# Kernel optimization log

Measured on AMD Instinct MI355X. Metric: run time of the kernel, lower is better.

Reference implementation:

```python
import jax, jax.numpy as jnp
import numpy as np

B, N, D = 16, 1024, 768
H = 12
HD = D // H
HID = 4 * D
EPS = 1e-6


def _layernorm(x, g, b):
    mu = jnp.mean(x, axis=-1, keepdims=True)
    var = jnp.mean(jnp.square(x - mu), axis=-1, keepdims=True)
    return (x - mu) * jax.lax.rsqrt(var + EPS) * g + b


def setup_inputs() -> dict:
    key = jax.random.key(0)
    ks = jax.random.split(key, 8)
    s_d = 1.0 / np.sqrt(D)
    s_h = 1.0 / np.sqrt(HID)
    return {
        "x": jax.random.normal(ks[0], (B, N, D), dtype=jnp.float32),
        "qkv_w": jax.random.uniform(ks[1], (3 * D, D), jnp.float32, -s_d, s_d),
        "proj_w": jax.random.uniform(ks[2], (D, D), jnp.float32, -s_d, s_d),
        "proj_b": jax.random.uniform(ks[3], (D,), jnp.float32, -s_d, s_d),
        "fc1_w": jax.random.uniform(ks[4], (HID, D), jnp.float32, -s_d, s_d),
        "fc1_b": jax.random.uniform(ks[5], (HID,), jnp.float32, -s_d, s_d),
        "fc2_w": jax.random.uniform(ks[6], (D, HID), jnp.float32, -s_h, s_h),
        "fc2_b": jax.random.uniform(ks[7], (D,), jnp.float32, -s_h, s_h),
        "norm1_g": jnp.ones((D,), jnp.float32),
        "norm1_b": jnp.zeros((D,), jnp.float32),
        "norm2_g": jnp.ones((D,), jnp.float32),
        "norm2_b": jnp.zeros((D,), jnp.float32),
    }


def _attention(x, qkv_w, proj_w, proj_b):
    b, n, _ = x.shape
    qkv = x @ qkv_w.T                                  # [b,n,3D] (no bias: qkv_bias=False)
    qkv = qkv.reshape(b, n, 3, H, HD)
    q, k, v = (jnp.transpose(qkv[:, :, i], (0, 2, 1, 3)) for i in range(3))  # [b,h,n,hd]
    scale = HD ** (-0.5)
    dots = jnp.einsum("bhid,bhjd->bhij", q, k) * scale
    attn = jax.nn.softmax(dots, axis=-1)
    out = jnp.einsum("bhij,bhjd->bhid", attn, v)
    out = jnp.transpose(out, (0, 2, 1, 3)).reshape(b, n, H * HD)
    return out @ proj_w.T + proj_b


def _mlp(x, fc1_w, fc1_b, fc2_w, fc2_b):
    h = jax.nn.gelu(x @ fc1_w.T + fc1_b, approximate=False)
    return h @ fc2_w.T + fc2_b


def reference(x, qkv_w, proj_w, proj_b, fc1_w, fc1_b, fc2_w, fc2_b,
              norm1_g, norm1_b, norm2_g, norm2_b):
    x = x + _attention(_layernorm(x, norm1_g, norm1_b), qkv_w, proj_w, proj_b)
    x = x + _mlp(_layernorm(x, norm2_g, norm2_b), fc1_w, fc1_b, fc2_w, fc2_b)
    return x
```

## Files before the change

### kernel.cpp

```cpp
#include <hip/hip_runtime.h>
#include <hip/hip_bf16.h>
#include <math.h>

using bf16 = __hip_bfloat16;
typedef __attribute__((ext_vector_type(8))) short short8;
typedef __attribute__((ext_vector_type(4))) short shortx4;
typedef __attribute__((ext_vector_type(4))) float floatx4;

#define BB 16
#define NN 1024
#define DD 768
#define HH 12
#define HD 64
#define HID 3072

#define QSCALE 0.1803368801f

__device__ __forceinline__ floatx4 mfma_bf16(short8 a, short8 b, floatx4 c) {
  return __builtin_amdgcn_mfma_f32_16x16x32_bf16(a, b, c, 0, 0, 0);
}

__device__ __forceinline__ short bf16_bits(float f) {
  union { bf16 h; short s; } u;
  u.h = __float2bfloat16(f);
  return u.s;
}

__device__ __forceinline__ void async_copy16(const void* g, void* l) {
  __builtin_amdgcn_global_load_lds(
      (const __attribute__((address_space(1))) unsigned int*)g,
      (__attribute__((address_space(3))) unsigned int*)l,
      16, 0, 0);
}

__device__ __forceinline__ float gelu_f(float x) {
  const float z = x * fmaf(0.10294324f, x * x, 2.3022082f);
  const float e = exp2f(z);
  return x - x * __builtin_amdgcn_rcpf(e + 1.0f);
}

__global__ __launch_bounds__(256)
void cvt_kernel(const float* __restrict__ in, bf16* __restrict__ out, int n4)
{
  const int i = blockIdx.x * 256 + threadIdx.x;
  if (i >= n4) return;
  const float4 v = ((const float4*)in)[i];
  shortx4 o;
  o.x = bf16_bits(v.x); o.y = bf16_bits(v.y);
  o.z = bf16_bits(v.z); o.w = bf16_bits(v.w);
  ((shortx4*)out)[i] = o;
}

__global__ __launch_bounds__(256)
void ln_kernel(const float* __restrict__ x, const float* __restrict__ g,
               const float* __restrict__ b, bf16* __restrict__ y)
{
  const int row = blockIdx.x;
  const int t = threadIdx.x;
  const float* xr = x + (size_t)row * DD;
  float v[3];
  float s = 0.f, s2 = 0.f;
#pragma unroll
  for (int i = 0; i < 3; ++i) {
    float f = xr[t + i * 256];
    v[i] = f;
    s += f;
    s2 += f * f;
  }
#pragma unroll
  for (int off = 1; off < 64; off <<= 1) {
    s  += __shfl_xor(s, off);
    s2 += __shfl_xor(s2, off);
  }
  __shared__ float red[2][4];
  const int wave = t >> 6, lane = t & 63;
  if (lane == 0) { red[0][wave] = s; red[1][wave] = s2; }
  __syncthreads();
  s  = red[0][0] + red[0][1] + red[0][2] + red[0][3];
  s2 = red[1][0] + red[1][1] + red[1][2] + red[1][3];
  const float mu = s * (1.f / DD);
  const float var = s2 * (1.f / DD) - mu * mu;
  const float inv = rsqrtf(var + 1e-6f);
  bf16* yr = y + (size_t)row * DD;
#pragma unroll
  for (int i = 0; i < 3; ++i) {
    int c = t + i * 256;
    yr[c] = __float2bfloat16((v[i] - mu) * inv * g[c] + b[c]);
  }
}

template <int EPI>
__global__ __launch_bounds__(256, 4)
void gemm_kernel(const bf16* __restrict__ A, const bf16* __restrict__ W,
                 const float* __restrict__ bias, const float* __restrict__ res,
                 void* __restrict__ Cv, int N, int K)
{
  __shared__ __align__(16) short smem[16896];
  short* sA = smem;
  short* sB = smem + 8192;

  const int tid  = threadIdx.x;
  const int lane = tid & 63;
  const int wave = tid >> 6;
  const int wm = wave & 1, wn = wave >> 1;
  const int row16 = lane & 15, quad = lane >> 4;

  const int lin = blockIdx.y * gridDim.x + blockIdx.x;
  const int per = gridDim.x * 8;
  const int pan = lin / per, rem = lin % per;
  const int bm = (pan * 8 + (rem & 7)) * 128;
  const int bn = (rem >> 3) * 128;

  const int lrow = lane >> 3;
  const int lkc  = (lane & 7) ^ lrow;

  const bf16* Ag = A + (size_t)(bm + wave * 32 + lrow) * K + lkc * 8;
  const bf16* Bg = W + (size_t)(bn + wave * 32 + lrow) * K + lkc * 8;
  short* sAw = sA + wave * 2048;
  short* sBw = sB + wave * 2048;

  floatx4 acc[4][4] = {};

  for (int kt = 0; kt < K; kt += 64) {
#pragma unroll
    for (int g = 0; g < 4; ++g) {
      async_copy16(Ag + (size_t)g * 8 * K + kt, sAw + g * 512);
      async_copy16(Bg + (size_t)g * 8 * K + kt, sBw + g * 512);
    }
    __syncthreads();
#pragma unroll
    for (int c = 0; c < 2; ++c) {
      short8 af[4], bfr[4];
      const int kc = c * 4 + quad;
#pragma unroll
      for (int mt = 0; mt < 4; ++mt) {
        const int row = wm * 64 + mt * 16 + row16;
        af[mt] = *(const short8*)&sA[(row >> 3) * 512 + ((row & 7) * 8 + (kc ^ (row & 7))) * 8];
      }
#pragma unroll
      for (int nt = 0; nt < 4; ++nt) {
        const int row = wn * 64 + nt * 16 + row16;
        bfr[nt] = *(const short8*)&sB[(row >> 3) * 512 + ((row & 7) * 8 + (kc ^ (row & 7))) * 8];
      }
#pragma unroll
      for (int mt = 0; mt < 4; ++mt)
#pragma unroll
        for (int nt = 0; nt < 4; ++nt)
          acc[mt][nt] = mfma_bf16(bfr[nt], af[mt], acc[mt][nt]);
    }
    __syncthreads();
  }

  if (EPI == 1) {
#pragma unroll
    for (int mt = 0; mt < 4; ++mt) {
      const int row = bm + wm * 64 + mt * 16 + row16;
#pragma unroll
      for (int nt = 0; nt < 4; ++nt) {
        const int col = bn + wn * 64 + nt * 16 + quad * 4;
        const floatx4 bv = *(const floatx4*)&bias[col];
        const floatx4 rv = *(const floatx4*)&res[(size_t)row * N + col];
        floatx4 o;
#pragma unroll
        for (int r = 0; r < 4; ++r) o[r] = acc[mt][nt][r] + bv[r] + rv[r];
        *(floatx4*)&((float*)Cv)[(size_t)row * N + col] = o;
      }
    }
  } else {
    short* sC = smem;
#pragma unroll
    for (int mt = 0; mt < 4; ++mt) {
      const int lr = wm * 64 + mt * 16 + row16;
#pragma unroll
      for (int nt = 0; nt < 4; ++nt) {
        const int lc = wn * 64 + nt * 16 + quad * 4;
        floatx4 bv = {};
        if (EPI == 2) bv = *(const floatx4*)&bias[bn + lc];
        shortx4 pk;
#pragma unroll
        for (int r = 0; r < 4; ++r) {
          float v = acc[mt][nt][r] + bv[r];
          if (EPI == 2) v = gelu_f(v);
          if (EPI == 0 && bn + lc < DD) v *= QSCALE;
          pk[r] = bf16_bits(v);
        }
        *(shortx4*)&sC[lr * 132 + lc] = pk;
      }
    }
    __syncthreads();
#pragma unroll
    for (int it = 0; it < 8; ++it) {
      const int row = (tid >> 4) + it * 16;
      const int col = (tid & 15) * 8;
      short8 v = *(const short8*)&sC[row * 132 + col];
      *(short8*)&((bf16*)Cv)[(size_t)(bm + row) * N + bn + col] = v;
    }
  }
}

__global__ __launch_bounds__(256)
void vtrans_kernel(const bf16* __restrict__ qkv, bf16* __restrict__ vt)
{
  const int bh = blockIdx.y;
  const int b = bh / HH, h = bh % HH;
  const int n0 = blockIdx.x * 64;
  __shared__ __align__(16) short tile[64 * 72];
  const int tid = threadIdx.x;

  const int r = tid >> 2, c16 = (tid & 3) * 16;
  const bf16* src = qkv + (size_t)(b * NN + n0 + r) * 2304 + 2 * DD + h * 64 + c16;
  *(short8*)&tile[r * 72 + c16]     = *(const short8*)(src);
  *(short8*)&tile[r * 72 + c16 + 8] = *(const short8*)(src + 8);
  __syncthreads();

#pragma unroll
  for (int it = 0; it < 2; ++it) {
    const int d  = (tid >> 3) + it * 32;
    const int jg = (tid & 7) * 8;
    short8 o;
#pragma unroll
    for (int t = 0; t < 8; ++t) ((short*)&o)[t] = tile[(jg + t) * 72 + d];
    *(short8*)&vt[((size_t)bh * 64 + d) * NN + n0 + jg] = o;
  }
}

__global__ __launch_bounds__(256, 2)
void attn_kernel(const bf16* __restrict__ qkv, const bf16* __restrict__ vt,
                 bf16* __restrict__ out)
{
  const int nbh = gridDim.y;
  int bh, qi;
  if ((nbh & 7) == 0) {
    const int lin = blockIdx.y * 8 + blockIdx.x;
    const int xcd = lin & 7;
    const int w   = lin >> 3;
    bh = xcd * (nbh >> 3) + (w >> 3);
    qi = w & 7;
  } else {
    bh = blockIdx.y; qi = blockIdx.x;
  }
  const int b = bh / HH, h = bh % HH;
  const int q0 = qi * 128;
  const int tid = threadIdx.x;
  const int lane = tid & 63;
  const int wave = tid >> 6;
  const int row16 = lane & 15, quad = lane >> 4;

  __shared__ __align__(16) short sK[4096];
  __shared__ __align__(16) short sVt[4096];
  __shared__ __align__(16) short sP[4][2][1024];

  const bf16* base  = qkv + (size_t)b * NN * 2304 + h * 64;
  const bf16* vbase = vt + (size_t)bh * 64 * NN;

  short8 qf[2][2];
#pragma unroll
  for (int qg = 0; qg < 2; ++qg) {
    const bf16* qrow = base + (size_t)(q0 + wave * 32 + qg * 16 + row16) * 2304;
    qf[qg][0] = *(const short8*)(qrow + quad * 8);
    qf[qg][1] = *(const short8*)(qrow + 32 + quad * 8);
  }

  floatx4 o_acc[2][4] = {};
  floatx4 l_acc[2] = {};
  const short8 ones = { (short)0x3F80, (short)0x3F80, (short)0x3F80, (short)0x3F80,
                        (short)0x3F80, (short)0x3F80, (short)0x3F80, (short)0x3F80 };

  const bf16* ksrc = base + DD + (size_t)(wave * 16 + row16) * 2304 + quad * 8;
  const bf16* vsrc = vbase + (size_t)(wave * 16 + row16) * NN + quad * 8;
  short* kdst = sK + wave * 1024 + lane * 8;
  short* vdst = sVt + wave * 1024 + lane * 8;

  async_copy16(ksrc, kdst);
  async_copy16(ksrc + 32, kdst + 512);
  async_copy16(vsrc, vdst);
  async_copy16(vsrc + 32, vdst + 512);

  for (int jt = 0; jt < NN / 64; ++jt) {
    __syncthreads();

    short8 vb[4][2];
#pragma unroll
    for (int dt = 0; dt < 4; ++dt) {
      vb[dt][0] = *(const short8*)&sVt[dt * 1024 + lane * 8];
      vb[dt][1] = *(const short8*)&sVt[dt * 1024 + 512 + lane * 8];
    }
    short8 kb[4][2];
#pragma unroll
    for (int nt = 0; nt < 4; ++nt) {
      kb[nt][0] = *(const short8*)&sK[nt * 1024 + lane * 8];
      kb[nt][1] = *(const short8*)&sK[nt * 1024 + 512 + lane * 8];
    }
    __syncthreads();

    if (jt + 1 < NN / 64) {
      const bf16* k2 = ksrc + (size_t)(jt + 1) * 64 * 2304;
      const bf16* v2 = vsrc + (jt + 1) * 64;
      async_copy16(k2, kdst);
      async_copy16(k2 + 32, kdst + 512);
      async_copy16(v2, vdst);
      async_copy16(v2 + 32, vdst + 512);
    }

#pragma unroll
    for (int nt = 0; nt < 4; ++nt) {
#pragma unroll
      for (int qg = 0; qg < 2; ++qg) {
        floatx4 st = {};
        st = mfma_bf16(kb[nt][0], qf[qg][0], st);
        st = mfma_bf16(kb[nt][1], qf[qg][1], st);
        const float e0 = exp2f(fminf(st[0], 30.f));
        const float e1 = exp2f(fminf(st[1], 30.f));
        const float e2 = exp2f(fminf(st[2], 30.f));
        const float e3 = exp2f(fminf(st[3], 30.f));
        union { __hip_bfloat162 h2[2]; shortx4 s4; } pu;
        pu.h2[0] = __float22bfloat162_rn(make_float2(e0, e1));
        pu.h2[1] = __float22bfloat162_rn(make_float2(e2, e3));
        *(shortx4*)&sP[wave][qg][(row16 + 16 * (2 * nt + (quad >> 1))) * 8 +
                                 (quad & 1) * 4] = pu.s4;
      }
    }

#pragma unroll
    for (int qg = 0; qg < 2; ++qg) {
      const short8 pf0 = *(const short8*)&sP[wave][qg][lane * 8];
      const short8 pf1 = *(const short8*)&sP[wave][qg][512 + lane * 8];
      l_acc[qg] = mfma_bf16(pf0, ones, l_acc[qg]);
      l_acc[qg] = mfma_bf16(pf1, ones, l_acc[qg]);
#pragma unroll
      for (int dt = 0; dt < 4; ++dt) {
        o_acc[qg][dt] = mfma_bf16(pf0, vb[dt][0], o_acc[qg][dt]);
        o_acc[qg][dt] = mfma_bf16(pf1, vb[dt][1], o_acc[qg][dt]);
      }
    }
  }

#pragma unroll
  for (int qg = 0; qg < 2; ++qg) {
#pragma unroll
    for (int r = 0; r < 4; ++r) {
      const float inv = 1.f / l_acc[qg][r];
      const size_t n = (size_t)(b * NN + q0 + wave * 32 + qg * 16 + quad * 4 + r);
#pragma unroll
      for (int dt = 0; dt < 4; ++dt) {
        out[n * DD + h * 64 + dt * 16 + row16] =
            __float2bfloat16(o_acc[qg][dt][r] * inv);
      }
    }
  }
}

extern "C" void kernel_launch(void* const* d_in, const int* in_sizes, int n_in,
                              void* d_out, int out_size, void* d_ws, size_t ws_size,
                              hipStream_t stream)
{
  const float* x       = (const float*)d_in[0];
  const float* qkv_w   = (const float*)d_in[1];
  const float* proj_w  = (const float*)d_in[2];
  const float* proj_b  = (const float*)d_in[3];
  const float* fc1_w   = (const float*)d_in[4];
  const float* fc1_b   = (const float*)d_in[5];
  const float* fc2_w   = (const float*)d_in[6];
  const float* fc2_b   = (const float*)d_in[7];
  const float* norm1_g = (const float*)d_in[8];
  const float* norm1_b = (const float*)d_in[9];
  const float* norm2_g = (const float*)d_in[10];
  const float* norm2_b = (const float*)d_in[11];
  float* out = (float*)d_out;

  const int M = BB * NN;
  char* ws = (char*)d_ws;

  bf16* wq = (bf16*)ws;
  bf16* wp = wq + (size_t)3 * DD * DD;
  bf16* w1 = wp + (size_t)DD * DD;
  bf16* w2 = w1 + (size_t)HID * DD;
  bf16* xn = w2 + (size_t)DD * HID;
  char* p2 = (char*)(xn + (size_t)M * DD);
  const size_t base_b = (size_t)(p2 - ws);

  int NBc = 1;
  for (int c = 16; c >= 1; c >>= 1)
    if (ws_size >= base_b + (size_t)c * 1024 * 7680) { NBc = c; break; }

  const int Rc = NBc * NN;
  bf16* qkvb = (bf16*)p2;
  bf16* aob  = qkvb + (size_t)Rc * 2304;
  bf16* vtb  = aob  + (size_t)Rc * DD;
  bf16* hb   = (bf16*)p2;

  cvt_kernel<<<(3 * DD * DD / 4 + 255) / 256, 256, 0, stream>>>(qkv_w, wq, 3 * DD * DD / 4);
  cvt_kernel<<<(DD * DD / 4 + 255) / 256, 256, 0, stream>>>(proj_w, wp, DD * DD / 4);
  cvt_kernel<<<(HID * DD / 4 + 255) / 256, 256, 0, stream>>>(fc1_w, w1, HID * DD / 4);
  cvt_kernel<<<(DD * HID / 4 + 255) / 256, 256, 0, stream>>>(fc2_w, w2, DD * HID / 4);

  ln_kernel<<<M, 256, 0, stream>>>(x, norm1_g, norm1_b, xn);

  for (int c = 0; c < BB / NBc; ++c) {
    const size_t r0 = (size_t)c * Rc;
    gemm_kernel<0><<<dim3(3 * DD / 128, Rc / 128), 256, 0, stream>>>(
        xn + r0 * DD, wq, nullptr, nullptr, qkvb, 3 * DD, DD);
    vtrans_kernel<<<dim3(NN / 64, NBc * HH), 256, 0, stream>>>(qkvb, vtb);
    attn_kernel<<<dim3(NN / 128, NBc * HH), 256, 0, stream>>>(qkvb, vtb, aob);
    gemm_kernel<1><<<dim3(DD / 128, Rc / 128), 256, 0, stream>>>(
        aob, wp, proj_b, x + r0 * DD, out + r0 * DD, DD, DD);
  }

  ln_kernel<<<M, 256, 0, stream>>>(out, norm2_g, norm2_b, xn);

  for (int c = 0; c < BB / NBc; ++c) {
    const size_t r0 = (size_t)c * Rc;
    gemm_kernel<2><<<dim3(HID / 128, Rc / 128), 256, 0, stream>>>(
        xn + r0 * DD, w1, fc1_b, nullptr, hb, HID, DD);
    gemm_kernel<1><<<dim3(DD / 128, Rc / 128), 256, 0, stream>>>(
        hb, w2, fc2_b, out + r0 * DD, out + r0 * DD, DD, HID);
  }
}
```

Measured before the change: 558.0 us.

## Double-buffer K/V tiles in attention to remove second barrier per iteration

```diff
diff --git a/kernel.cpp b/kernel.cpp
--- a/kernel.cpp
+++ b/kernel.cpp
@@ -246,8 +246,8 @@
   const int wave = tid >> 6;
   const int row16 = lane & 15, quad = lane >> 4;
 
-  __shared__ __align__(16) short sK[4096];
-  __shared__ __align__(16) short sVt[4096];
+  __shared__ __align__(16) short sK[2][4096];
+  __shared__ __align__(16) short sVt[2][4096];
   __shared__ __align__(16) short sP[4][2][1024];
 
   const bf16* base  = qkv + (size_t)b * NN * 2304 + h * 64;
@@ -268,47 +268,37 @@
 
   const bf16* ksrc = base + DD + (size_t)(wave * 16 + row16) * 2304 + quad * 8;
   const bf16* vsrc = vbase + (size_t)(wave * 16 + row16) * NN + quad * 8;
-  short* kdst = sK + wave * 1024 + lane * 8;
-  short* vdst = sVt + wave * 1024 + lane * 8;
-
-  async_copy16(ksrc, kdst);
-  async_copy16(ksrc + 32, kdst + 512);
-  async_copy16(vsrc, vdst);
-  async_copy16(vsrc + 32, vdst + 512);
+  const int dofs = wave * 1024 + lane * 8;
+
+  async_copy16(ksrc, &sK[0][dofs]);
+  async_copy16(ksrc + 32, &sK[0][dofs + 512]);
+  async_copy16(vsrc, &sVt[0][dofs]);
+  async_copy16(vsrc + 32, &sVt[0][dofs + 512]);
 
   for (int jt = 0; jt < NN / 64; ++jt) {
     __syncthreads();
-
-    short8 vb[4][2];
-#pragma unroll
-    for (int dt = 0; dt < 4; ++dt) {
-      vb[dt][0] = *(const short8*)&sVt[dt * 1024 + lane * 8];
-      vb[dt][1] = *(const short8*)&sVt[dt * 1024 + 512 + lane * 8];
-    }
-    short8 kb[4][2];
-#pragma unroll
-    for (int nt = 0; nt < 4; ++nt) {
-      kb[nt][0] = *(const short8*)&sK[nt * 1024 + lane * 8];
-      kb[nt][1] = *(const short8*)&sK[nt * 1024 + 512 + lane * 8];
-    }
-    __syncthreads();
-
+    const int cur = jt & 1;
     if (jt + 1 < NN / 64) {
+      const int nxt = cur ^ 1;
       const bf16* k2 = ksrc + (size_t)(jt + 1) * 64 * 2304;
       const bf16* v2 = vsrc + (jt + 1) * 64;
-      async_copy16(k2, kdst);
-      async_copy16(k2 + 32, kdst + 512);
-      async_copy16(v2, vdst);
-      async_copy16(v2 + 32, vdst + 512);
-    }
+      async_copy16(k2, &sK[nxt][dofs]);
+      async_copy16(k2 + 32, &sK[nxt][dofs + 512]);
+      async_copy16(v2, &sVt[nxt][dofs]);
+      async_copy16(v2 + 32, &sVt[nxt][dofs + 512]);
+    }
+    const short* sKc = sK[cur];
+    const short* sVc = sVt[cur];
 
 #pragma unroll
     for (int nt = 0; nt < 4; ++nt) {
+      const short8 kb0 = *(const short8*)&sKc[nt * 1024 + lane * 8];
+      const short8 kb1 = *(const short8*)&sKc[nt * 1024 + 512 + lane * 8];
 #pragma unroll
       for (int qg = 0; qg < 2; ++qg) {
         floatx4 st = {};
-        st = mfma_bf16(kb[nt][0], qf[qg][0], st);
-        st = mfma_bf16(kb[nt][1], qf[qg][1], st);
+        st = mfma_bf16(kb0, qf[qg][0], st);
+        st = mfma_bf16(kb1, qf[qg][1], st);
         const float e0 = exp2f(fminf(st[0], 30.f));
         const float e1 = exp2f(fminf(st[1], 30.f));
         const float e2 = exp2f(fminf(st[2], 30.f));
@@ -321,16 +311,24 @@
       }
     }
 
+    __builtin_amdgcn_sched_barrier(0);
+
+    short8 pf[2][2];
 #pragma unroll
     for (int qg = 0; qg < 2; ++qg) {
-      const short8 pf0 = *(const short8*)&sP[wave][qg][lane * 8];
-      const short8 pf1 = *(const short8*)&sP[wave][qg][512 + lane * 8];
-      l_acc[qg] = mfma_bf16(pf0, ones, l_acc[qg]);
-      l_acc[qg] = mfma_bf16(pf1, ones, l_acc[qg]);
-#pragma unroll
-      for (int dt = 0; dt < 4; ++dt) {
-        o_acc[qg][dt] = mfma_bf16(pf0, vb[dt][0], o_acc[qg][dt]);
-        o_acc[qg][dt] = mfma_bf16(pf1, vb[dt][1], o_acc[qg][dt]);
+      pf[qg][0] = *(const short8*)&sP[wave][qg][lane * 8];
+      pf[qg][1] = *(const short8*)&sP[wave][qg][512 + lane * 8];
+      l_acc[qg] = mfma_bf16(pf[qg][0], ones, l_acc[qg]);
+      l_acc[qg] = mfma_bf16(pf[qg][1], ones, l_acc[qg]);
+    }
+#pragma unroll
+    for (int dt = 0; dt < 4; ++dt) {
+      const short8 vb0 = *(const short8*)&sVc[dt * 1024 + lane * 8];
+      const short8 vb1 = *(const short8*)&sVc[dt * 1024 + 512 + lane * 8];
+#pragma unroll
+      for (int qg = 0; qg < 2; ++qg) {
+        o_acc[qg][dt] = mfma_bf16(pf[qg][0], vb0, o_acc[qg][dt]);
+        o_acc[qg][dt] = mfma_bf16(pf[qg][1], vb1, o_acc[qg][dt]);
       }
     }
   }
```

After: 560.8 us. About the same (+0.5%).
